# Kernel tuning notes

Measured on AMD Instinct MI355X. Metric: run time of the kernel, lower is better.

Reference implementation:

```python
import jax, jax.numpy as jnp
import numpy as np

H, DH = 12, 64
EPS = 1e-6
ROPE_BASE = 100.0

def rms_norm(x, scale=None, eps=EPS):
    xf = x.astype(jnp.float32)
    n = xf * jax.lax.rsqrt(jnp.mean(xf * xf, axis=-1, keepdims=True) + eps)
    if scale is not None:
        n = n * scale.astype(jnp.float32)
    return n.astype(x.dtype)

def rotate_half(x):
    h = x.shape[-1] // 2
    return jnp.concatenate([-x[..., h:], x[..., :h]], axis=-1)

def rope_cos_sin(pos_ids, head_dim, base=ROPE_BASE):
    # pos_ids: [B, N, 2] int -> cos/sin [B, N, head_dim]
    dim = head_dim // 2
    inv = 1.0 / base ** (jnp.arange(0, dim, 2, dtype=jnp.float32) / dim)  # [dim//2]
    cos_l, sin_l = [], []
    for i in range(2):  # x and y coordinate
        pos = pos_ids[:, :, i].astype(jnp.float32)           # [B, N]
        freqs = pos[:, :, None] * inv[None, None, :]          # [B, N, dim//2]
        emb = jnp.concatenate([freqs, freqs], axis=-1)        # [B, N, dim]
        cos_l.append(jnp.cos(emb))
        sin_l.append(jnp.sin(emb))
    return jnp.concatenate(cos_l, axis=-1), jnp.concatenate(sin_l, axis=-1)

def apply_2d_rope(x, cos, sin):
    # x: [B, N, H, Dh]; cos/sin: [B, N, Dh]; split channels evenly between x/y.
    c = x.shape[-1] // 2
    outs = []
    for k in range(2):
        xs = x[..., k * c:(k + 1) * c]
        cc = cos[:, :, None, k * c:(k + 1) * c]
        ss = sin[:, :, None, k * c:(k + 1) * c]
        outs.append(xs * cc + rotate_half(xs) * ss)
    return jnp.concatenate(outs, axis=-1)

def setup_inputs() -> dict:
    key = jax.random.key(0)
    ks = jax.random.split(key, 7)
    B, N, D = 8, 1024, 768
    hidden_states = jax.random.normal(ks[0], (B, N, D), dtype=jnp.float32)
    pixel_position_ids = jax.random.randint(ks[1], (B, N, 2), 0, 32, dtype=jnp.int32)
    s = 0.02
    Wq = jax.random.normal(ks[2], (H * DH, D), dtype=jnp.float32) * s
    Wk = jax.random.normal(ks[3], (H * DH, D), dtype=jnp.float32) * s
    Wv = jax.random.normal(ks[4], (H * DH, D), dtype=jnp.float32) * s
    Wo = jax.random.normal(ks[5], (D, H * DH), dtype=jnp.float32) * s
    q_scale = jnp.ones((DH,), dtype=jnp.float32)
    k_scale = jnp.ones((DH,), dtype=jnp.float32)
    return {"hidden_states": hidden_states, "pixel_position_ids": pixel_position_ids,
            "Wq": Wq, "Wk": Wk, "Wv": Wv, "Wo": Wo,
            "q_scale": q_scale, "k_scale": k_scale}

def reference(hidden_states, pixel_position_ids, Wq, Wk, Wv, Wo, q_scale, k_scale):
    B, N, D = hidden_states.shape
    # QKV projections (clip bounds are +/-inf -> no-op). Weights are [out, in].
    q = (hidden_states @ Wq.T).reshape(B, N, H, DH)
    k = (hidden_states @ Wk.T).reshape(B, N, H, DH)
    v = (hidden_states @ Wv.T).reshape(B, N, H, DH)
    # Per-head RMSNorm (v has no learned scale)
    q = rms_norm(q, q_scale)
    k = rms_norm(k, k_scale)
    v = rms_norm(v, None)
    # 2D RoPE
    cos, sin = rope_cos_sin(pixel_position_ids, DH)
    q = apply_2d_rope(q, cos, sin)
    k = apply_2d_rope(k, cos, sin)
    # Full attention, scaling = 1.0, softmax in fp32
    scores = jnp.einsum('bqhd,bkhd->bhqk', q, k)
    attn = jax.nn.softmax(scores.astype(jnp.float32), axis=-1).astype(q.dtype)
    out = jnp.einsum('bhqk,bkhd->bqhd', attn, v).reshape(B, N, H * DH)
    return out @ Wo.T
```

## Files before the change

kernel.cpp:

```cpp
#include <hip/hip_runtime.h>

typedef _Float16 f16;
typedef __attribute__((ext_vector_type(8))) _Float16 f16x8;
typedef __attribute__((ext_vector_type(4))) _Float16 f16x4;
typedef __attribute__((ext_vector_type(4))) float f32x4;

#define NH 12
#define DHD 64
#define NB 8
#define NSEQ 1024
#define DMODEL 768
#define BHN (NB*NH)
#define ROWS_PER (BHN*NSEQ)

#define MFMA(a,b,c) __builtin_amdgcn_mfma_f32_16x16x32_f16(a,b,c,0,0,0)

__device__ __forceinline__ void gload16(const void* g, void* l) {
  __builtin_amdgcn_global_load_lds(
      (__attribute__((address_space(1))) void*)(g),
      (__attribute__((address_space(3))) void*)(l), 16, 0, 0);
}

__global__ __launch_bounds__(256) void cast_kernel(const float* __restrict__ in,
                                                   f16* __restrict__ out, int n) {
  int i = (blockIdx.x * blockDim.x + threadIdx.x) * 4;
  if (i < n) {
    float4 v = *(const float4*)(in + i);
    f16x4 o = {(f16)v.x, (f16)v.y, (f16)v.z, (f16)v.w};
    *(f16x4*)(out + i) = o;
  }
}

__global__ __launch_bounds__(256) void cast_w_kernel(const float* __restrict__ Wq,
                                                     const float* __restrict__ Wk,
                                                     const float* __restrict__ Wv,
                                                     const float* __restrict__ Wo,
                                                     f16* __restrict__ Wf,
                                                     f16* __restrict__ Wof,
                                                     float2* __restrict__ rtab, int nw) {
  int i = (blockIdx.x * blockDim.x + threadIdx.x) * 4;
  if (i < 4*nw) {
    int which = i / nw;
    int off = i - which*nw;
    const float* src = (which == 0) ? Wq : (which == 1) ? Wk : (which == 2) ? Wv : Wo;
    f16* dst = (which < 3) ? (Wf + (size_t)which*nw + off) : (Wof + off);
    float4 v = *(const float4*)(src + off);
    f16x4 o = {(f16)v.x, (f16)v.y, (f16)v.z, (f16)v.w};
    *(f16x4*)dst = o;
  }
  if (blockIdx.x == 0) {
    for (int e = threadIdx.x; e < 512; e += 256) {
      int pos = e >> 4, k = e & 15;
      float ang = (float)pos * __expf((float)k * (-4.605170185988091f / 16.0f));
      float sn, cs;
      __sincosf(ang, &sn, &cs);
      rtab[e] = make_float2(cs, sn);
    }
  }
}

template<int MODE>
__global__ __launch_bounds__(256) void gemm_bt(const f16* __restrict__ A,
                                               const f16* __restrict__ B,
                                               float* __restrict__ Cout,
                                               f16* __restrict__ QKout,
                                               f16* __restrict__ Vout,
                                               const int* __restrict__ pos_ids,
                                               const float* __restrict__ q_scale,
                                               const float* __restrict__ k_scale,
                                               const float2* __restrict__ rtab,
                                               int M, int N, int K) {
  constexpr int BN = (MODE == 1) ? 128 : 64;
  constexpr int NJ = BN / 32;
  constexpr int ABUF = 8192;
  constexpr int BBUF = BN*64;
  __shared__ __align__(16) f16 SH[2*ABUF + 2*BBUF];
  const int tid = threadIdx.x;
  const int w = tid >> 6, l = tid & 63;
  const int wr = w >> 1, wc = w & 1;
  const int g = l >> 4, i16 = l & 15;

  int bx, by;
  {
    int id = blockIdx.x;
    const int nbx = (MODE == 1) ? 18 : 12;
    const int chunk = (MODE == 1) ? 144 : 96;
    int idp = (id & 7) * chunk + (id >> 3);
    by = idp / nbx; bx = idp - by * nbx;
  }
  const bool isV = (MODE == 1) && (bx >= 12);

  const f32x4 fzero = {0.f, 0.f, 0.f, 0.f};
  f32x4 acc[4][NJ];
#pragma unroll
  for (int i = 0; i < 4; i++)
#pragma unroll
    for (int j = 0; j < NJ; j++) acc[i][j] = fzero;

  const int srow = tid >> 3;
  const int schunk = (tid & 7) ^ (srow & 7);
  const size_t arow = (size_t)(by*128 + srow)*K + schunk*8;
  const size_t brow = (size_t)(bx*BN + srow)*K + schunk*8;

  const int nt = K / 64;
#define STAGE(buf, k0)                                                          \
  {                                                                             \
    char* AlB = (char*)(SH + (buf)*ABUF) + w*1024;                              \
    char* BlB = (char*)(SH + 2*ABUF + (buf)*BBUF) + w*1024;                     \
    _Pragma("unroll")                                                           \
    for (int n = 0; n < 4; ++n)                                                 \
      gload16(A + arow + (size_t)(n*32)*K + (k0), AlB + n*4096);                \
    _Pragma("unroll")                                                           \
    for (int n = 0; n < BN/32; ++n)                                             \
      gload16(B + brow + (size_t)(n*32)*K + (k0), BlB + n*4096);                \
  }

  STAGE(0, 0);
  __syncthreads();
  for (int t = 0; t < nt; ++t) {
    const int buf = t & 1;
    if (t + 1 < nt) STAGE(buf ^ 1, (t + 1)*64);
    const f16* Ac = SH + buf*ABUF;
    const f16* Bc = SH + 2*ABUF + buf*BBUF;
#pragma unroll
    for (int kk = 0; kk < 2; ++kk) {
      f16x8 af[4], bfr[NJ];
#pragma unroll
      for (int i = 0; i < 4; i++)
        af[i] = *(const f16x8*)(Ac + (wr*64 + i*16 + i16)*64 + ((kk*4 + g) ^ (i16 & 7))*8);
#pragma unroll
      for (int j = 0; j < NJ; j++)
        bfr[j] = *(const f16x8*)(Bc + (wc*(BN/2) + j*16 + i16)*64 + ((kk*4 + g) ^ (i16 & 7))*8);
#pragma unroll
      for (int i = 0; i < 4; i++)
#pragma unroll
        for (int j = 0; j < NJ; j++)
          acc[i][j] = MFMA(af[i], bfr[j], acc[i][j]);
    }
    __syncthreads();
  }
#undef STAGE

  const int m0 = by*128 + wr*64;
  const int n0 = bx*BN + wc*(BN/2);
  if (MODE == 0) {
#pragma unroll
    for (int i = 0; i < 4; i++)
#pragma unroll
      for (int j = 0; j < NJ; j++)
#pragma unroll
        for (int r = 0; r < 4; r++) {
          int m = m0 + i*16 + g*4 + r;
          int n = n0 + j*16 + i16;
          Cout[(size_t)m*N + n] = acc[i][j][r];
        }
  } else if (isV) {
    const int h0 = (bx - 12)*2;
    const int bb = by >> 3;
    const int ns0 = (by & 7) * 128;
    f16* Lt = SH;
#pragma unroll
    for (int i = 0; i < 4; i++) {
      f32x4 ssv = fzero;
#pragma unroll
      for (int j = 0; j < 4; j++)
#pragma unroll
        for (int r = 0; r < 4; r++) ssv[r] += acc[i][j][r]*acc[i][j][r];
#pragma unroll
      for (int d = 1; d < 16; d <<= 1)
#pragma unroll
        for (int r = 0; r < 4; r++) ssv[r] += __shfl_xor(ssv[r], d);
#pragma unroll
      for (int r = 0; r < 4; r++) {
        float rinv = rsqrtf(ssv[r] * (1.0f/64.0f) + 1e-6f);
        int nsl = wr*64 + i*16 + g*4 + r;
#pragma unroll
        for (int j = 0; j < 4; j++)
          Lt[(wc*64 + j*16 + i16)*136 + nsl] = (f16)(acc[i][j][r]*rinv);
      }
    }
    __syncthreads();
    const int dh = tid >> 1, half = tid & 1;
    f16* dst = Vout + ((size_t)((bb*NH + h0 + (dh >> 6))*64 + (dh & 63)))*1024
               + ns0 + half*64;
    const f16* ls = Lt + dh*136 + half*64;
#pragma unroll
    for (int e = 0; e < 8; ++e)
      *(uint4*)(dst + e*8) = *(const uint4*)(ls + e*8);
  } else {
    const int qkv = n0 / DMODEL;
    const int h = (n0 - qkv*DMODEL) >> 6;
    const float* scp = (qkv == 0) ? q_scale : k_scale;
    float scl[4];
#pragma unroll
    for (int j = 0; j < 4; j++) scl[j] = scp[j*16 + i16];
    const float2* rt = rtab + i16;
#pragma unroll
    for (int i = 0; i < 4; i++) {
      f32x4 ssv = fzero;
#pragma unroll
      for (int j = 0; j < 4; j++)
#pragma unroll
        for (int r = 0; r < 4; r++) ssv[r] += acc[i][j][r]*acc[i][j][r];
#pragma unroll
      for (int d = 1; d < 16; d <<= 1)
#pragma unroll
        for (int r = 0; r < 4; r++) ssv[r] += __shfl_xor(ssv[r], d);
#pragma unroll
      for (int r = 0; r < 4; r++) {
        int m = m0 + i*16 + g*4 + r;
        int bb = m >> 10, ns = m & 1023;
        float rinv = rsqrtf(ssv[r] * (1.0f/64.0f) + 1e-6f);
        int2 pp = *(const int2*)(pos_ids + ((size_t)bb*NSEQ + ns)*2);
        float2 t0 = rt[pp.x*16];
        float2 t1 = rt[pp.y*16];
        float x0 = acc[i][0][r]*rinv*scl[0];
        float x1 = acc[i][1][r]*rinv*scl[1];
        float x2 = acc[i][2][r]*rinv*scl[2];
        float x3 = acc[i][3][r]*rinv*scl[3];
        size_t row = ((size_t)qkv*BHN + bb*NH + h)*NSEQ + ns;
        f16* ob = QKout + row*64;
        ob[i16]      = (f16)(x0*t0.x - x1*t0.y);
        ob[16 + i16] = (f16)(x1*t0.x + x0*t0.y);
        ob[32 + i16] = (f16)(x2*t1.x - x3*t1.y);
        ob[48 + i16] = (f16)(x3*t1.x + x2*t1.y);
      }
    }
  }
}

__device__ __forceinline__ int sigma_perm(int p) {
  return (p & 0x20) | ((p & 0xC) << 1) | ((p & 0x10) >> 2) | (p & 3);
}

__global__ __launch_bounds__(256) void attn_kernel(const f16* __restrict__ QKu,
                                                   const f16* __restrict__ Vtu,
                                                   f16* __restrict__ O) {
  const int bh = blockIdx.y;
  const int q0 = blockIdx.x * 64;
  const int tid = threadIdx.x, w = tid >> 6, l = tid & 63;
  const int g = l >> 4, i16 = l & 15;
  const int g4 = g*4;
  const int sw = i16 & 7;
  const int b = bh / NH, h = bh - b*NH;

  __shared__ __align__(16) f16 Ks[2*64*64];
  __shared__ __align__(16) f16 Vs[2*64*64];

  const f16* qrow = QKu + ((size_t)bh*NSEQ + q0 + w*16 + i16)*64;
  f16x8 q0f = *(const f16x8*)(qrow + g*8);
  f16x8 q1f = *(const f16x8*)(qrow + 32 + g*8);

  const char* Kb  = (const char*)(QKu + (size_t)(BHN + bh)*NSEQ*64);
  const char* Vtb = (const char*)(Vtu + (size_t)bh*64*1024);
  const int prow0 = w*8 + (l >> 3);
  const int cl = (l & 7) ^ (l >> 3);
  const char* Ksrc0 = Kb + sigma_perm(prow0)*128 + cl*16;
  const char* Ksrc1 = Kb + (sigma_perm(prow0) + 32)*128 + cl*16;
  const char* Vsrc0 = Vtb + prow0*2048 + cl*16;
  const char* Vsrc1 = Vtb + (prow0 + 32)*2048 + cl*16;

  const f32x4 fzero = {0.f, 0.f, 0.f, 0.f};
  float mR = -1e30f, lR = 0.f;
  f32x4 o[4];
#pragma unroll
  for (int t = 0; t < 4; t++) o[t] = fzero;

  int cur = 0;
  {
    char* kd = (char*)Ks + w*1024;
    char* vd = (char*)Vs + w*1024;
    gload16(Ksrc0, kd);
    gload16(Ksrc1, kd + 4096);
    gload16(Vsrc0, vd);
    gload16(Vsrc1, vd + 4096);
  }
  __syncthreads();

  for (int t = 0; t < 16; ++t) {
    if (t < 15) {
      char* kd = (char*)Ks + (cur^1)*8192 + w*1024;
      char* vd = (char*)Vs + (cur^1)*8192 + w*1024;
      gload16(Ksrc0 + (t+1)*8192, kd);
      gload16(Ksrc1 + (t+1)*8192, kd + 4096);
      gload16(Vsrc0 + (t+1)*128,  vd);
      gload16(Vsrc1 + (t+1)*128,  vd + 4096);
    }
    const f16* Kc = Ks + cur*4096;
    const f16* Vc = Vs + cur*4096;

    f32x4 s[4] = {fzero, fzero, fzero, fzero};
    __builtin_amdgcn_s_setprio(1);
#pragma unroll
    for (int j = 0; j < 4; ++j) {
      const f16* kr = Kc + (j*16 + i16)*64;
      f16x8 k0 = *(const f16x8*)(kr + (g ^ sw)*8);
      f16x8 k1 = *(const f16x8*)(kr + ((g^4) ^ sw)*8);
      s[j] = MFMA(k0, q0f, s[j]);
      s[j] = MFMA(k1, q1f, s[j]);
    }
    __builtin_amdgcn_s_setprio(0);

    float tm = fmaxf(
        fmaxf(fmaxf(fmaxf(s[0][0],s[0][1]), fmaxf(s[0][2],s[0][3])),
              fmaxf(fmaxf(s[1][0],s[1][1]), fmaxf(s[1][2],s[1][3]))),
        fmaxf(fmaxf(fmaxf(s[2][0],s[2][1]), fmaxf(s[2][2],s[2][3])),
              fmaxf(fmaxf(s[3][0],s[3][1]), fmaxf(s[3][2],s[3][3]))));
    tm = fmaxf(tm, __shfl_xor(tm, 16));
    tm = fmaxf(tm, __shfl_xor(tm, 32));
    if (__any(tm > mR + 8.0f)) {
      float nm = fmaxf(mR, tm);
      float fac = __expf(mR - nm);
      mR = nm;
      lR *= fac;
#pragma unroll
      for (int r = 0; r < 4; ++r) {
        float fr = __shfl(fac, g4 + r);
        o[0][r] *= fr; o[1][r] *= fr; o[2][r] *= fr; o[3][r] *= fr;
      }
    }
    float rs = 0.f;
#pragma unroll
    for (int j = 0; j < 4; ++j)
#pragma unroll
      for (int r = 0; r < 4; ++r) { s[j][r] = __expf(s[j][r] - mR); rs += s[j][r]; }
    rs += __shfl_xor(rs, 16);
    rs += __shfl_xor(rs, 32);
    lR += rs;

    f16x8 pa0, pa1;
#pragma unroll
    for (int e = 0; e < 4; ++e) {
      pa0[e]   = (f16)s[0][e];
      pa0[4+e] = (f16)s[1][e];
      pa1[e]   = (f16)s[2][e];
      pa1[4+e] = (f16)s[3][e];
    }
    __builtin_amdgcn_s_setprio(1);
#pragma unroll
    for (int t2 = 0; t2 < 4; ++t2) {
      const f16* vr = Vc + (t2*16 + i16)*64;
      f16x8 bv0 = *(const f16x8*)(vr + (g ^ sw)*8);
      f16x8 bv1 = *(const f16x8*)(vr + ((g^4) ^ sw)*8);
      o[t2] = MFMA(pa0, bv0, o[t2]);
      o[t2] = MFMA(pa1, bv1, o[t2]);
    }
    __builtin_amdgcn_s_setprio(0);

    __syncthreads();
    cur ^= 1;
  }

#pragma unroll
  for (int r = 0; r < 4; ++r) {
    float lr = __shfl(lR, g4 + r);
    float invl = 1.0f / lr;
    int q = q0 + w*16 + g4 + r;
    size_t base = ((size_t)(b*NSEQ + q))*DMODEL + h*DHD;
#pragma unroll
    for (int t2 = 0; t2 < 4; ++t2)
      O[base + t2*16 + i16] = (f16)(o[t2][r] * invl);
  }
}

extern "C" void kernel_launch(void* const* d_in, const int* in_sizes, int n_in,
                              void* d_out, int out_size, void* d_ws, size_t ws_size,
                              hipStream_t stream) {
  const float* hs = (const float*)d_in[0];
  const int*   pos = (const int*)d_in[1];
  const float* Wq = (const float*)d_in[2];
  const float* Wk = (const float*)d_in[3];
  const float* Wv = (const float*)d_in[4];
  const float* Wo = (const float*)d_in[5];
  const float* qs = (const float*)d_in[6];
  const float* ks = (const float*)d_in[7];

  const int nhs = 8192*768;
  const int nw  = 768*768;

  char* p = (char*)d_ws;
  f16* Xf   = (f16*)p; p += (size_t)nhs*2;
  f16* Wf   = (f16*)p; p += (size_t)3*nw*2;
  f16* Wof  = (f16*)p; p += (size_t)nw*2;
  f16* QKpk = (f16*)p; p += (size_t)2*ROWS_PER*64*2;
  f16* Vt   = (f16*)p; p += (size_t)ROWS_PER*64*2;
  f16* Ob   = (f16*)p; p += (size_t)nhs*2;
  float2* Rtab = (float2*)p; p += 512*sizeof(float2);

  cast_kernel<<<nhs/1024, 256, 0, stream>>>(hs, Xf, nhs);
  cast_w_kernel<<<(4*nw)/1024, 256, 0, stream>>>(Wq, Wk, Wv, Wo, Wf, Wof, Rtab, nw);

  gemm_bt<1><<<1152, 256, 0, stream>>>(Xf, Wf, nullptr, QKpk, Vt,
                                       pos, qs, ks, Rtab, 8192, 2304, 768);
  attn_kernel<<<dim3(16, 96), 256, 0, stream>>>(QKpk, Vt, Ob);
  gemm_bt<0><<<768, 256, 0, stream>>>(Ob, Wof, (float*)d_out, nullptr, nullptr,
                                      nullptr, nullptr, nullptr, nullptr, 8192, 768, 768);
}
```

Baseline: 136.4 us.

## Fold log2e into Q scale, use exp2, MFMA row-sum, packed f16 converts

Folds log2(e) into the Q RMSNorm scale so the attention softmax can use the native exp2 instead of __expf, with the lazy-rescale threshold adjusted to match. The per-row softmax denominator is now accumulated by two extra MFMAs against a ones vector, replacing the shuffle reductions. Probability conversion to f16 uses packed round-toward-zero converts, and the max reduction is regrouped into three-input max ops. This cuts VALU and shuffle work in the attention inner loop at the cost of two extra MFMAs per tile and slightly different rounding.

```diff
diff --git a/kernel.cpp b/kernel.cpp
--- a/kernel.cpp
+++ b/kernel.cpp
@@ -3,6 +3,7 @@
 typedef _Float16 f16;
 typedef __attribute__((ext_vector_type(8))) _Float16 f16x8;
 typedef __attribute__((ext_vector_type(4))) _Float16 f16x4;
+typedef __attribute__((ext_vector_type(2))) __fp16 h16x2;
 typedef __attribute__((ext_vector_type(4))) float f32x4;
 
 #define NH 12
@@ -88,7 +89,6 @@
     int idp = (id & 7) * chunk + (id >> 3);
     by = idp / nbx; bx = idp - by * nbx;
   }
-  const bool isV = (MODE == 1) && (bx >= 12);
 
   const f32x4 fzero = {0.f, 0.f, 0.f, 0.f};
   f32x4 acc[4][NJ];
@@ -143,7 +143,7 @@
 
   const int m0 = by*128 + wr*64;
   const int n0 = bx*BN + wc*(BN/2);
-  if (MODE == 0) {
+  if constexpr (MODE == 0) {
 #pragma unroll
     for (int i = 0; i < 4; i++)
 #pragma unroll
@@ -154,7 +154,8 @@
           int n = n0 + j*16 + i16;
           Cout[(size_t)m*N + n] = acc[i][j][r];
         }
-  } else if (isV) {
+  } else {
+  if (bx >= 12) {
     const int h0 = (bx - 12)*2;
     const int bb = by >> 3;
     const int ns0 = (by & 7) * 128;
@@ -193,7 +194,10 @@
     const float* scp = (qkv == 0) ? q_scale : k_scale;
     float scl[4];
 #pragma unroll
-    for (int j = 0; j < 4; j++) scl[j] = scp[j*16 + i16];
+    for (int j = 0; j < 4; j++) {
+      scl[j] = scp[j*16 + i16];
+      if (qkv == 0) scl[j] *= 1.4426950408889634f;
+    }
     const float2* rt = rtab + i16;
 #pragma unroll
     for (int i = 0; i < 4; i++) {
@@ -227,11 +231,14 @@
       }
     }
   }
+  }
 }
 
 __device__ __forceinline__ int sigma_perm(int p) {
   return (p & 0x20) | ((p & 0xC) << 1) | ((p & 0x10) >> 2) | (p & 3);
 }
+
+#define FM3(a,b,c) fmaxf(fmaxf(a,b),c)
 
 __global__ __launch_bounds__(256) void attn_kernel(const f16* __restrict__ QKu,
                                                    const f16* __restrict__ Vtu,
@@ -261,8 +268,11 @@
   const char* Vsrc1 = Vtb + (prow0 + 32)*2048 + cl*16;
 
   const f32x4 fzero = {0.f, 0.f, 0.f, 0.f};
-  float mR = -1e30f, lR = 0.f;
+  const f16x8 vones = {(f16)1.f,(f16)1.f,(f16)1.f,(f16)1.f,
+                       (f16)1.f,(f16)1.f,(f16)1.f,(f16)1.f};
+  float mR = -1e30f;
   f32x4 o[4];
+  f32x4 acc_l = fzero;
 #pragma unroll
   for (int t = 0; t < 4; t++) o[t] = fzero;
 
@@ -301,41 +311,41 @@
     }
     __builtin_amdgcn_s_setprio(0);
 
-    float tm = fmaxf(
-        fmaxf(fmaxf(fmaxf(s[0][0],s[0][1]), fmaxf(s[0][2],s[0][3])),
-              fmaxf(fmaxf(s[1][0],s[1][1]), fmaxf(s[1][2],s[1][3]))),
-        fmaxf(fmaxf(fmaxf(s[2][0],s[2][1]), fmaxf(s[2][2],s[2][3])),
-              fmaxf(fmaxf(s[3][0],s[3][1]), fmaxf(s[3][2],s[3][3]))));
+    float t0m = FM3(s[0][0], s[0][1], s[0][2]);
+    float t1m = FM3(s[0][3], s[1][0], s[1][1]);
+    float t2m = FM3(s[1][2], s[1][3], s[2][0]);
+    float t3m = FM3(s[2][1], s[2][2], s[2][3]);
+    float t4m = FM3(s[3][0], s[3][1], s[3][2]);
+    float tm = fmaxf(FM3(FM3(t0m, t1m, t2m), t3m, t4m), s[3][3]);
     tm = fmaxf(tm, __shfl_xor(tm, 16));
     tm = fmaxf(tm, __shfl_xor(tm, 32));
-    if (__any(tm > mR + 8.0f)) {
+    if (__any(tm > mR + 11.5416f)) {
       float nm = fmaxf(mR, tm);
-      float fac = __expf(mR - nm);
+      float fac = __builtin_amdgcn_exp2f(mR - nm);
       mR = nm;
-      lR *= fac;
 #pragma unroll
       for (int r = 0; r < 4; ++r) {
         float fr = __shfl(fac, g4 + r);
         o[0][r] *= fr; o[1][r] *= fr; o[2][r] *= fr; o[3][r] *= fr;
+        acc_l[r] *= fr;
       }
     }
-    float rs = 0.f;
 #pragma unroll
     for (int j = 0; j < 4; ++j)
 #pragma unroll
-      for (int r = 0; r < 4; ++r) { s[j][r] = __expf(s[j][r] - mR); rs += s[j][r]; }
-    rs += __shfl_xor(rs, 16);
-    rs += __shfl_xor(rs, 32);
-    lR += rs;
-
-    f16x8 pa0, pa1;
-#pragma unroll
-    for (int e = 0; e < 4; ++e) {
-      pa0[e]   = (f16)s[0][e];
-      pa0[4+e] = (f16)s[1][e];
-      pa1[e]   = (f16)s[2][e];
-      pa1[4+e] = (f16)s[3][e];
-    }
+      for (int r = 0; r < 4; ++r) s[j][r] = __builtin_amdgcn_exp2f(s[j][r] - mR);
+
+    union { h16x2 h[4]; f16x8 v; } u0, u1;
+    u0.h[0] = __builtin_amdgcn_cvt_pkrtz(s[0][0], s[0][1]);
+    u0.h[1] = __builtin_amdgcn_cvt_pkrtz(s[0][2], s[0][3]);
+    u0.h[2] = __builtin_amdgcn_cvt_pkrtz(s[1][0], s[1][1]);
+    u0.h[3] = __builtin_amdgcn_cvt_pkrtz(s[1][2], s[1][3]);
+    u1.h[0] = __builtin_amdgcn_cvt_pkrtz(s[2][0], s[2][1]);
+    u1.h[1] = __builtin_amdgcn_cvt_pkrtz(s[2][2], s[2][3]);
+    u1.h[2] = __builtin_amdgcn_cvt_pkrtz(s[3][0], s[3][1]);
+    u1.h[3] = __builtin_amdgcn_cvt_pkrtz(s[3][2], s[3][3]);
+    f16x8 pa0 = u0.v, pa1 = u1.v;
+
     __builtin_amdgcn_s_setprio(1);
 #pragma unroll
     for (int t2 = 0; t2 < 4; ++t2) {
@@ -345,6 +355,8 @@
       o[t2] = MFMA(pa0, bv0, o[t2]);
       o[t2] = MFMA(pa1, bv1, o[t2]);
     }
+    acc_l = MFMA(pa0, vones, acc_l);
+    acc_l = MFMA(pa1, vones, acc_l);
     __builtin_amdgcn_s_setprio(0);
 
     __syncthreads();
@@ -353,8 +365,7 @@
 
 #pragma unroll
   for (int r = 0; r < 4; ++r) {
-    float lr = __shfl(lR, g4 + r);
-    float invl = 1.0f / lr;
+    float invl = 1.0f / acc_l[r];
     int q = q0 + w*16 + g4 + r;
     size_t base = ((size_t)(b*NSEQ + q))*DMODEL + h*DHD;
 #pragma unroll
```

Measured after the change: 131.2 us. 3.8% less time.
